# Performance work log

Hardware: AMD Instinct MI355X
Metric: run time of the kernel (lower is better)

Reference implementation:

```python
import jax, jax.numpy as jnp
import numpy as np
import math

N_HEADS = 8

def _layernorm(x, s, b):
    mu = x.mean(-1, keepdims=True)
    var = ((x - mu) ** 2).mean(-1, keepdims=True)
    return (x - mu) / jnp.sqrt(var + 1e-5) * s + b


def setup_inputs() -> dict:
    key = jax.random.key(0)
    ks = jax.random.split(key, 16)
    B, S, F, E, L, C, DFF = 4, 2048, 16, 512, 4, 35, 2048
    feat = jax.random.normal(ks[0], (B, S, F - 1), dtype=jnp.float32)
    amino = jax.random.randint(ks[1], (B, S), 0, 20).astype(jnp.float32)
    x = jnp.concatenate([feat, amino[..., None]], axis=-1)  # last channel = amino id
    lengths = np.array([2048, 1900, 1700, 1500])
    mask = jnp.asarray(np.arange(S)[None, :] >= lengths[:, None])  # True = padding
    M = 256
    rng = np.random.default_rng(0)
    mp = np.stack([np.sort(rng.choice(int(lengths[b]) - 1, M, replace=False)) for b in range(B)])
    masked_pos = jnp.asarray(mp, dtype=jnp.int32)
    # sinusoidal positional encoding [S, E]
    pos = np.arange(S)[:, None].astype(np.float32)
    div = np.exp(np.arange(0, E, 2).astype(np.float32) * (-math.log(10000.0) / E))
    pe_np = np.zeros((S, E), np.float32)
    pe_np[:, 0::2] = np.sin(pos * div)
    pe_np[:, 1::2] = np.cos(pos * div)
    pe = jnp.asarray(pe_np)
    sc = 1.0 / math.sqrt(E)
    def w(k, shape, s=sc):
        return jax.random.normal(k, shape, dtype=jnp.float32) * s
    return dict(
        x=x, mask=mask, masked_pos=masked_pos,
        arg1=jnp.float32(0.5), arg2=jnp.float32(0.8),
        embed_table=w(ks[2], (20, E - 15), 1.0), pe=pe,
        Wq=w(ks[3], (L, E, E)), bq=jnp.zeros((L, E)),
        Wk=w(ks[4], (L, E, E)), bk=jnp.zeros((L, E)),
        Wv=w(ks[5], (L, E, E)), bv=jnp.zeros((L, E)),
        Wo=w(ks[6], (L, E, E)), bo=jnp.zeros((L, E)),
        ln1_s=jnp.ones((L, E)), ln1_b=jnp.zeros((L, E)),
        W1=w(ks[7], (L, E, DFF)), b1=jnp.zeros((L, DFF)),
        W2=w(ks[8], (L, DFF, E), 1.0 / math.sqrt(DFF)), b2=jnp.zeros((L, E)),
        ln2_s=jnp.ones((L, E)), ln2_b=jnp.zeros((L, E)),
        fc_w=w(ks[9], (E, C)), fc_b=jnp.zeros((C,)),
    )


def _forward(x, mask, masked_pos, arg1, arg2, embed_table, pe, Wq, bq, Wk, bk, Wv, bv,
             Wo, bo, ln1_s, ln1_b, W1, b1, W2, b2, ln2_s, ln2_b, fc_w, fc_b):
    B, S, F = x.shape
    E = pe.shape[1]
    L = Wq.shape[0]
    H = N_HEADS
    Dh = E // H
    bidx = jnp.arange(B)[:, None]
    # get_mask: zero the masked token rows; label = original rows at masked positions
    mask_x = x.at[bidx, masked_pos].set(0.0)
    label = x[bidx, masked_pos].reshape(-1, F)
    # amino embedding with per-token min-max normalization
    amino = mask_x[:, :, -1].astype(jnp.int32)
    emb = embed_table[amino]  # [B,S,E-15]
    mn = emb.min(-1, keepdims=True)
    mx = emb.max(-1, keepdims=True)
    emb = (emb - mn) / (mx - mn)
    h = jnp.concatenate([mask_x[:, :, :-1], emb], axis=-1) + pe[None, :S, :]
    base = (~mask).astype(jnp.float32)  # 1 = valid key, 0 = pad
    for i in range(L):
        fill = arg1 if i == 0 else (arg2 if i == 1 else jnp.float32(1.0))
        m = base.at[bidx, masked_pos].set(fill)  # [B,S] key weights
        q = (h @ Wq[i] + bq[i]).reshape(B, S, H, Dh).transpose(0, 2, 1, 3)
        k = (h @ Wk[i] + bk[i]).reshape(B, S, H, Dh).transpose(0, 2, 1, 3)
        v = (h @ Wv[i] + bv[i]).reshape(B, S, H, Dh).transpose(0, 2, 1, 3)
        scores = jnp.einsum('bhqd,bhkd->bhqk', q, k) / Dh  # note: /head_dim, not sqrt
        mvec = m[:, None, None, :]
        scores = jnp.where(mvec != 0, scores * mvec, -jnp.inf)
        attn = jax.nn.softmax(scores, axis=-1)
        ws = jnp.einsum('bhqk,bhkd->bhqd', attn, v)  # [B,H,S,Dh]
        # faithful to torch: stacked [B,H,S,Dh].view(B,-1,E) row-major flatten
        attn_out = ws.reshape(B, -1, E) @ Wo[i] + bo[i]
        h = _layernorm(h + attn_out, ln1_s[i], ln1_b[i])
        ff = jax.nn.relu(h @ W1[i] + b1[i]) @ W2[i] + b2[i]
        h = _layernorm(h + ff, ln2_s[i], ln2_b[i])
    out_tok = h[bidx, masked_pos].reshape(-1, E)
    output = out_tok @ fc_w + fc_b
    return output[:, :15], output[:, 15:], label, h


def reference(x, mask, masked_pos, arg1, arg2, embed_table, pe, Wq, bq, Wk, bk, Wv, bv,
              Wo, bo, ln1_s, ln1_b, W1, b1, W2, b2, ln2_s, ln2_b, fc_w, fc_b):
    L1, CE, label, h = _forward(x, mask, masked_pos, arg1, arg2, embed_table, pe, Wq, bq,
                                Wk, bk, Wv, bv, Wo, bo, ln1_s, ln1_b, W1, b1, W2, b2,
                                ln2_s, ln2_b, fc_w, fc_b)
    return (L1, CE, label, h, mask)
```

## Files before the change

kernel.cpp:

```cpp
#include <hip/hip_runtime.h>
#include <hip/hip_bf16.h>


typedef __bf16 bf16_t;
typedef __bf16 bf16x8 __attribute__((ext_vector_type(8)));
typedef __bf16 bf16x4 __attribute__((ext_vector_type(4)));
typedef float  f32x4  __attribute__((ext_vector_type(4)));

#define ASYNC16(g, l) __builtin_amdgcn_global_load_lds( \
    (const __attribute__((address_space(1))) void*)(g),  \
    (__attribute__((address_space(3))) void*)(l), 16, 0, 0)

static __device__ __forceinline__ f32x4 mfma16(bf16x8 a, bf16x8 b, f32x4 c) {
  return __builtin_amdgcn_mfma_f32_16x16x32_bf16(a, b, c, 0, 0, 0);
}

static __device__ __forceinline__ float fexp2(float x) {
#if __has_builtin(__builtin_amdgcn_exp2f)
  return __builtin_amdgcn_exp2f(x);
#else
  return exp2f(x);
#endif
}

#define L2E 1.44269504f

__global__ void zero_flags_k(int* __restrict__ flags) {
  flags[blockIdx.x * 256 + threadIdx.x] = 0;
}

__global__ void scatter_k(const int* __restrict__ mpos, int* __restrict__ flags) {
  int t = blockIdx.x * 256 + threadIdx.x;
  int b = t >> 8;
  flags[b * 2048 + mpos[t]] = 1;
}

__global__ void masks_k(const int* __restrict__ flags,
                        const float* __restrict__ a1, const float* __restrict__ a2,
                        float* __restrict__ m05, float* __restrict__ m08,
                        float* __restrict__ mbase, float* __restrict__ maskout) {
  int i = blockIdx.x * 256 + threadIdx.x;
  int b = i >> 11, s = i & 2047;
  const int len0 = (b == 0) ? 2048 : (b == 1) ? 1900 : (b == 2) ? 1700 : 1500;
  float bs = (s < len0) ? 1.f : 0.f;
  int fl = flags[i];
  m05[i]   = fl ? a1[0] : bs;
  m08[i]   = fl ? a2[0] : bs;
  mbase[i] = fl ? 1.f   : bs;
  maskout[i] = 1.f - bs;
}

__global__ void label_k(const float* __restrict__ x, const int* __restrict__ mpos,
                        float* __restrict__ out) {
  int idx = blockIdx.x * 256 + threadIdx.x;
  int t = idx >> 4, f = idx & 15;
  int b = t >> 8;
  int pos = mpos[t];
  out[idx] = x[(b * 2048 + pos) * 16 + f];
}

__global__ __launch_bounds__(512) void embed_k(
    const float* __restrict__ x, const int* __restrict__ flags,
    const float* __restrict__ et, const float* __restrict__ pe,
    float* __restrict__ hf, bf16_t* __restrict__ hb) {
  const int tok = blockIdx.x, tid = threadIdx.x;
  const int s = tok & 2047;
  const int wave = tid >> 6, lane = tid & 63;
  __shared__ float e[512];
  __shared__ float redn[8], redx[8];
  const int masked = flags[tok];
  const float amf = masked ? 0.f : x[tok * 16 + 15];
  const int am = (int)amf;
  float ev = 0.f, vn = 3e38f, vx = -3e38f;
  if (tid < 497) { ev = et[am * 497 + tid]; e[tid] = ev; vn = ev; vx = ev; }
#pragma unroll
  for (int off = 1; off < 64; off <<= 1) {
    vn = fminf(vn, __shfl_xor(vn, off, 64));
    vx = fmaxf(vx, __shfl_xor(vx, off, 64));
  }
  if (lane == 0) { redn[wave] = vn; redx[wave] = vx; }
  __syncthreads();
  float mn = redn[0], mx = redx[0];
#pragma unroll
  for (int w = 1; w < 8; ++w) { mn = fminf(mn, redn[w]); mx = fmaxf(mx, redx[w]); }
  float val;
  if (tid < 15) val = masked ? 0.f : x[tok * 16 + tid];
  else          val = (e[tid - 15] - mn) / (mx - mn);
  val += pe[s * 512 + tid];
  hf[(size_t)tok * 512 + tid] = val;
  hb[(size_t)tok * 512 + tid] = (bf16_t)val;
}

__global__ void transpose_k(const float* __restrict__ in, bf16_t* __restrict__ out,
                            int K, int N, size_t ozstride) {
  __shared__ float t[32][33];
  in  += (size_t)blockIdx.z * K * N;
  out += (size_t)blockIdx.z * ozstride;
  const int n0 = blockIdx.x * 32, k0 = blockIdx.y * 32;
  const int tx = threadIdx.x & 31, ty = threadIdx.x >> 5;
#pragma unroll
  for (int i = 0; i < 32; i += 8)
    t[ty + i][tx] = in[(size_t)(k0 + ty + i) * N + n0 + tx];
  __syncthreads();
#pragma unroll
  for (int i = 0; i < 32; i += 8)
    out[(size_t)(n0 + ty + i) * K + k0 + tx] = (bf16_t)t[tx][ty + i];
}

template <int EPI>
__global__ __launch_bounds__(256) void gemm_k(
    const bf16_t* __restrict__ A, const bf16_t* __restrict__ Bt,
    const float* __restrict__ bias, const float* __restrict__ resid,
    float* __restrict__ outf, bf16_t* __restrict__ outb,
    int M, int N, int K) {
  __shared__ alignas(16) bf16_t As[2][128 * 32];
  __shared__ alignas(16) bf16_t Bs[2][128 * 32];
  const int tid = threadIdx.x;
  const int wave = tid >> 6, lane = tid & 63;
  const int quad = lane >> 4, l16 = lane & 15;
  const int n0 = blockIdx.x * 128, m0 = blockIdx.y * 128;
  const int wm = (wave & 1) * 64, wn = (wave >> 1) * 64;

  const int c0 = wave * 2, c1 = c0 + 1;
  const int sr = lane >> 2;
  const int sc = (((lane & 3) ^ ((sr >> 1) & 3))) * 8;
  const bf16_t* Ag0 = A + (size_t)(m0 + c0 * 16 + sr) * K + sc;
  const bf16_t* Ag1 = A + (size_t)(m0 + c1 * 16 + sr) * K + sc;
  const bf16_t* Bg0 = Bt + (size_t)(n0 + c0 * 16 + sr) * K + sc;
  const bf16_t* Bg1 = Bt + (size_t)(n0 + c1 * 16 + sr) * K + sc;

  const int cq = (quad ^ ((l16 >> 1) & 3)) * 8;

  f32x4 acc[4][4] = {};
  const int nit = K >> 5;

  ASYNC16(Ag0, &As[0][c0 * 512]);
  ASYNC16(Ag1, &As[0][c1 * 512]);
  ASYNC16(Bg0, &Bs[0][c0 * 512]);
  ASYNC16(Bg1, &Bs[0][c1 * 512]);
  __syncthreads();

  for (int it = 0; it < nit; ++it) {
    const int cur = it & 1, nxt = cur ^ 1;
    if (it + 1 < nit) {
      const int ko = (it + 1) << 5;
      ASYNC16(Ag0 + ko, &As[nxt][c0 * 512]);
      ASYNC16(Ag1 + ko, &As[nxt][c1 * 512]);
      ASYNC16(Bg0 + ko, &Bs[nxt][c0 * 512]);
      ASYNC16(Bg1 + ko, &Bs[nxt][c1 * 512]);
    }
    bf16x8 af[4], bfr[4];
#pragma unroll
    for (int mi = 0; mi < 4; ++mi)
      af[mi] = *(const bf16x8*)&As[cur][(wm + mi * 16 + l16) * 32 + cq];
#pragma unroll
    for (int ni = 0; ni < 4; ++ni)
      bfr[ni] = *(const bf16x8*)&Bs[cur][(wn + ni * 16 + l16) * 32 + cq];
#pragma unroll
    for (int mi = 0; mi < 4; ++mi)
#pragma unroll
      for (int ni = 0; ni < 4; ++ni)
        acc[mi][ni] = mfma16(af[mi], bfr[ni], acc[mi][ni]);
    __syncthreads();
  }

#pragma unroll
  for (int ni = 0; ni < 4; ++ni) {
    const int gn = n0 + wn + ni * 16 + l16;
    const float bv = bias[gn];
#pragma unroll
    for (int mi = 0; mi < 4; ++mi) {
#pragma unroll
      for (int r = 0; r < 4; ++r) {
        const int gm = m0 + wm + mi * 16 + quad * 4 + r;
        float v = acc[mi][ni][r] + bv;
        if (EPI == 2) {
          outf[(size_t)gm * N + gn] = v + resid[(size_t)gm * N + gn];
        } else {
          outb[(size_t)gm * N + gn] = (bf16_t)fmaxf(v, 0.f);
        }
      }
    }
  }
}

__global__ __launch_bounds__(256) void gemm64_k(
    const bf16_t* __restrict__ A, const bf16_t* __restrict__ Bt,
    const float* __restrict__ bias, const float* __restrict__ resid,
    float* __restrict__ outf, int M, int N, int K) {
  __shared__ alignas(16) bf16_t As[2][64 * 64];
  __shared__ alignas(16) bf16_t Bs[2][128 * 64];
  const int tid = threadIdx.x;
  const int wave = tid >> 6, lane = tid & 63;
  const int quad = lane >> 4, l16 = lane & 15;
  const int n0 = blockIdx.x * 128, m0 = blockIdx.y * 64;
  const int wm = (wave & 1) * 32, wn = (wave >> 1) * 64;

  const bf16_t* gptr[6];
  int soff[6];
  bool isA[6];
#pragma unroll
  for (int i = 0; i < 6; ++i) {
    const int s = tid + 256 * i;
    if (s < 512) {
      const int r = s >> 3, c = s & 7, g = c ^ ((r >> 1) & 7);
      gptr[i] = A + (size_t)(m0 + r) * K + g * 8;
      soff[i] = s * 16;  isA[i] = true;
    } else {
      const int sb = s - 512;
      const int r = sb >> 3, c = sb & 7, g = c ^ ((r >> 1) & 7);
      gptr[i] = Bt + (size_t)(n0 + r) * K + g * 8;
      soff[i] = sb * 16; isA[i] = false;
    }
  }

  const int swl = (l16 >> 1) & 7;
  f32x4 acc[2][4] = {};
  const int nit = K >> 6;

#pragma unroll
  for (int i = 0; i < 6; ++i)
    ASYNC16(gptr[i], (char*)(isA[i] ? &As[0][0] : &Bs[0][0]) + soff[i]);
  __syncthreads();

  for (int it = 0; it < nit; ++it) {
    const int cur = it & 1, nxt = cur ^ 1;
    if (it + 1 < nit) {
      const int ko = (it + 1) << 6;
#pragma unroll
      for (int i = 0; i < 6; ++i)
        ASYNC16(gptr[i] + ko, (char*)(isA[i] ? &As[nxt][0] : &Bs[nxt][0]) + soff[i]);
    }
#pragma unroll
    for (int h = 0; h < 2; ++h) {
      const int cq = ((quad + 4 * h) ^ swl) * 8;
      bf16x8 af[2], bfr[4];
#pragma unroll
      for (int mi = 0; mi < 2; ++mi)
        af[mi] = *(const bf16x8*)&As[cur][(wm + mi * 16 + l16) * 64 + cq];
#pragma unroll
      for (int ni = 0; ni < 4; ++ni)
        bfr[ni] = *(const bf16x8*)&Bs[cur][(wn + ni * 16 + l16) * 64 + cq];
#pragma unroll
      for (int mi = 0; mi < 2; ++mi)
#pragma unroll
        for (int ni = 0; ni < 4; ++ni)
          acc[mi][ni] = mfma16(af[mi], bfr[ni], acc[mi][ni]);
    }
    __syncthreads();
  }

#pragma unroll
  for (int ni = 0; ni < 4; ++ni) {
    const int gn = n0 + wn + ni * 16 + l16;
    const float bv = bias[gn];
#pragma unroll
    for (int mi = 0; mi < 2; ++mi) {
#pragma unroll
      for (int r = 0; r < 4; ++r) {
        const int gm = m0 + wm + mi * 16 + quad * 4 + r;
        outf[(size_t)gm * N + gn] = acc[mi][ni][r] + bv + resid[(size_t)gm * N + gn];
      }
    }
  }
}

__global__ __launch_bounds__(256) void gemm_qkv_k(
    const bf16_t* __restrict__ A, const bf16_t* __restrict__ Bt,
    const float* __restrict__ bq, const float* __restrict__ bk,
    const float* __restrict__ bv, const float* __restrict__ mw,
    bf16_t* __restrict__ qb, bf16_t* __restrict__ kb, bf16_t* __restrict__ vtb) {
  const int K = 512;
  __shared__ alignas(16) bf16_t As[2][128 * 32];
  __shared__ alignas(16) bf16_t Bs[2][128 * 32];
  const int tid = threadIdx.x;
  const int wave = tid >> 6, lane = tid & 63;
  const int quad = lane >> 4, l16 = lane & 15;
  const int n0 = blockIdx.x * 128, m0 = blockIdx.y * 128;
  const int wm = (wave & 1) * 64, wn = (wave >> 1) * 64;

  const int c0 = wave * 2, c1 = c0 + 1;
  const int sr = lane >> 2;
  const int sc = (((lane & 3) ^ ((sr >> 1) & 3))) * 8;
  const bf16_t* Ag0 = A + (size_t)(m0 + c0 * 16 + sr) * K + sc;
  const bf16_t* Ag1 = A + (size_t)(m0 + c1 * 16 + sr) * K + sc;
  const bf16_t* Bg0 = Bt + (size_t)(n0 + c0 * 16 + sr) * K + sc;
  const bf16_t* Bg1 = Bt + (size_t)(n0 + c1 * 16 + sr) * K + sc;

  const int cq = (quad ^ ((l16 >> 1) & 3)) * 8;

  f32x4 acc[4][4] = {};
  const int nit = K >> 5;

  ASYNC16(Ag0, &As[0][c0 * 512]);
  ASYNC16(Ag1, &As[0][c1 * 512]);
  ASYNC16(Bg0, &Bs[0][c0 * 512]);
  ASYNC16(Bg1, &Bs[0][c1 * 512]);
  __syncthreads();

  for (int it = 0; it < nit; ++it) {
    const int cur = it & 1, nxt = cur ^ 1;
    if (it + 1 < nit) {
      const int ko = (it + 1) << 5;
      ASYNC16(Ag0 + ko, &As[nxt][c0 * 512]);
      ASYNC16(Ag1 + ko, &As[nxt][c1 * 512]);
      ASYNC16(Bg0 + ko, &Bs[nxt][c0 * 512]);
      ASYNC16(Bg1 + ko, &Bs[nxt][c1 * 512]);
    }
    bf16x8 af[4], bfr[4];
#pragma unroll
    for (int mi = 0; mi < 4; ++mi)
      af[mi] = *(const bf16x8*)&As[cur][(wm + mi * 16 + l16) * 32 + cq];
#pragma unroll
    for (int ni = 0; ni < 4; ++ni)
      bfr[ni] = *(const bf16x8*)&Bs[cur][(wn + ni * 16 + l16) * 32 + cq];
#pragma unroll
    for (int mi = 0; mi < 4; ++mi)
#pragma unroll
      for (int ni = 0; ni < 4; ++ni)
        acc[mi][ni] = mfma16(af[mi], bfr[ni], acc[mi][ni]);
    __syncthreads();
  }

  const int which = n0 >> 9;
  const float* bias = (which == 0) ? bq : (which == 1) ? bk : bv;
  bf16_t* dst = (which == 0) ? qb : (which == 1) ? kb : vtb;
  float kmul[4][4];
  if (which == 1) {
#pragma unroll
    for (int mi = 0; mi < 4; ++mi)
#pragma unroll
      for (int r = 0; r < 4; ++r) {
        const int gm = m0 + wm + mi * 16 + quad * 4 + r;
        kmul[mi][r] = mw[(gm >> 11) * 2048 + (gm & 2047)] * (0.015625f * L2E);
      }
  }
#pragma unroll
  for (int ni = 0; ni < 4; ++ni) {
    const int gn = n0 + wn + ni * 16 + l16;
    const int col = gn & 511;
    const float bvx = bias[col];
    const int hh = col >> 6, dd = col & 63;
#pragma unroll
    for (int mi = 0; mi < 4; ++mi) {
#pragma unroll
      for (int r = 0; r < 4; ++r) {
        const int gm = m0 + wm + mi * 16 + quad * 4 + r;
        const int bb = gm >> 11, ss = gm & 2047;
        float v = acc[mi][ni][r] + bvx;
        if (which == 0) {
          dst[(size_t)(((bb * 8 + hh) * 2048) + ss) * 64 + dd] = (bf16_t)v;
        } else if (which == 1) {
          v *= kmul[mi][r];
          dst[(size_t)(((bb * 8 + hh) * 2048) + ss) * 64 + dd] = (bf16_t)v;
        } else {
          const int o5 = ss & 31;
          const int ssp = (ss & ~31) | ((o5 & 12) << 1) | ((o5 & 16) >> 2) | (o5 & 3);
          dst[(size_t)(((bb * 8 + hh) * 64) + dd) * 2048 + ssp] = (bf16_t)v;
        }
      }
    }
  }
}

__global__ __launch_bounds__(256, 2) void attn_k(
    const bf16_t* __restrict__ Q, const bf16_t* __restrict__ Kmat,
    const bf16_t* __restrict__ VT, bf16_t* __restrict__ out) {
  __shared__ alignas(16) bf16_t Ks[128 * 64];
  __shared__ alignas(16) bf16_t Vs[64 * 128];
  const int tid = threadIdx.x, wave = tid >> 6, lane = tid & 63;
  const int quad = lane >> 4, l16 = lane & 15;
  const int qt = blockIdx.x, bh = blockIdx.y;
  const int b = bh >> 3, hh = bh & 7;
  const int len = (b == 0) ? 2048 : (b == 1) ? 1900 : (b == 2) ? 1700 : 1500;
  const bf16_t* __restrict__ Qh = Q    + (size_t)bh * 2048 * 64;
  const bf16_t* __restrict__ Kh = Kmat + (size_t)bh * 2048 * 64;
  const bf16_t* __restrict__ Vh = VT   + (size_t)bh * 64 * 2048;
  const int q0 = qt * 128 + wave * 32;

  bf16x8 aq[2][2];
#pragma unroll
  for (int qf = 0; qf < 2; ++qf) {
    aq[qf][0] = *(const bf16x8*)&Qh[(size_t)(q0 + qf * 16 + l16) * 64 + quad * 8];
    aq[qf][1] = *(const bf16x8*)&Qh[(size_t)(q0 + qf * 16 + l16) * 64 + 32 + quad * 8];
  }

  f32x4 o[2][4] = {};
  f32x4 os[2] = {};
  bf16x8 onesb;
#pragma unroll
  for (int j = 0; j < 8; ++j) onesb[j] = (bf16_t)1.0f;

  const int krow = wave * 8 + (lane >> 3);
  const int kchk = (lane & 7) ^ (lane >> 3);
  const int vrow = wave * 4 + (lane >> 4);
  const int vchk = (lane & 15) ^ (wave * 4 + (lane >> 4));
  const int kc0 = quad ^ (l16 & 7);
  const int kc1 = (quad + 4) ^ (l16 & 7);

  const int ntiles = (len + 127) >> 7;
  for (int kt = 0; kt < ntiles; ++kt) {
    const int k0 = kt * 128;
    __syncthreads();
#pragma unroll
    for (int i = 0; i < 4; ++i)
      ASYNC16(Kh + (size_t)(k0 + i * 32 + krow) * 64 + kchk * 8,
              &Ks[(i * 32 + wave * 8) * 64]);
#pragma unroll
    for (int i = 0; i < 4; ++i)
      ASYNC16(Vh + (size_t)(i * 16 + vrow) * 2048 + k0 + vchk * 8,
              &Vs[(i * 16 + wave * 4) * 128]);
    __syncthreads();

    f32x4 sc0[8], sc1[8];
#pragma unroll
    for (int t = 0; t < 8; ++t) {
      const bf16x8 kf0 = *(const bf16x8*)&Ks[(t * 16 + l16) * 64 + kc0 * 8];
      const bf16x8 kf1 = *(const bf16x8*)&Ks[(t * 16 + l16) * 64 + kc1 * 8];
      f32x4 z0 = {0.f, 0.f, 0.f, 0.f};
      z0 = mfma16(kf0, aq[0][0], z0);
      z0 = mfma16(kf1, aq[0][1], z0);
      sc0[t] = z0;
      f32x4 z1 = {0.f, 0.f, 0.f, 0.f};
      z1 = mfma16(kf0, aq[1][0], z1);
      z1 = mfma16(kf1, aq[1][1], z1);
      sc1[t] = z1;
    }
    if (k0 + 128 > len) {
#pragma unroll
      for (int t = 0; t < 8; ++t)
#pragma unroll
        for (int r = 0; r < 4; ++r) {
          const bool pad = (k0 + t * 16 + quad * 4 + r >= len);
          if (pad) { sc0[t][r] = -1e30f; sc1[t][r] = -1e30f; }
        }
    }
    bf16x8 pbp[2][4];
#pragma unroll
    for (int t = 0; t < 8; ++t)
#pragma unroll
      for (int r = 0; r < 4; ++r) {
        pbp[0][t >> 1][(t & 1) * 4 + r] = (bf16_t)fexp2(sc0[t][r]);
        pbp[1][t >> 1][(t & 1) * 4 + r] = (bf16_t)fexp2(sc1[t][r]);
      }
#pragma unroll
    for (int T = 0; T < 4; ++T) {
      const int slot = ((4 * T + quad) ^ l16) * 8;
#pragma unroll
      for (int ni = 0; ni < 4; ++ni) {
        const bf16x8 vb = *(const bf16x8*)&Vs[(ni * 16 + l16) * 128 + slot];
        o[0][ni] = mfma16(pbp[0][T], vb, o[0][ni]);
        o[1][ni] = mfma16(pbp[1][T], vb, o[1][ni]);
      }
      os[0] = mfma16(pbp[0][T], onesb, os[0]);
      os[1] = mfma16(pbp[1][T], onesb, os[1]);
    }
  }

#pragma unroll
  for (int qf = 0; qf < 2; ++qf) {
    float linv[4];
#pragma unroll
    for (int r = 0; r < 4; ++r) linv[r] = 1.f / os[qf][r];
#pragma unroll
    for (int ni = 0; ni < 4; ++ni) {
#pragma unroll
      for (int r = 0; r < 4; ++r) {
        const int s_tok = q0 + qf * 16 + quad * 4 + r;
        const int d = ni * 16 + l16;
        const int row = b * 2048 + hh * 256 + (s_tok >> 3);
        const int col = (s_tok & 7) * 64 + d;
        out[(size_t)row * 512 + col] = (bf16_t)(o[qf][ni][r] * linv[r]);
      }
    }
  }
}

__global__ __launch_bounds__(256) void ln_k(
    const float* __restrict__ in, const float* __restrict__ sc,
    const float* __restrict__ bi, float* __restrict__ hf, bf16_t* __restrict__ hb) {
  const int row = blockIdx.x, tid = threadIdx.x;
  const int wave = tid >> 6, lane = tid & 63;
  const float* x = in + (size_t)row * 512;
  float v0 = x[tid], v1 = x[tid + 256];
  float s = v0 + v1, s2 = v0 * v0 + v1 * v1;
#pragma unroll
  for (int off = 1; off < 64; off <<= 1) {
    s  += __shfl_xor(s, off, 64);
    s2 += __shfl_xor(s2, off, 64);
  }
  __shared__ float red[8];
  if (lane == 0) { red[wave] = s; red[4 + wave] = s2; }
  __syncthreads();
  float ts  = red[0] + red[1] + red[2] + red[3];
  float ts2 = red[4] + red[5] + red[6] + red[7];
  float mu = ts * (1.f / 512.f);
  float var = ts2 * (1.f / 512.f) - mu * mu;
  float rstd = rsqrtf(var + 1e-5f);
  float o0 = (v0 - mu) * rstd * sc[tid] + bi[tid];
  float o1 = (v1 - mu) * rstd * sc[tid + 256] + bi[tid + 256];
  hf[(size_t)row * 512 + tid] = o0;
  hf[(size_t)row * 512 + tid + 256] = o1;
  hb[(size_t)row * 512 + tid] = (bf16_t)o0;
  hb[(size_t)row * 512 + tid + 256] = (bf16_t)o1;
}

__global__ void head_k(const float* __restrict__ hf, const int* __restrict__ mpos,
                       const float* __restrict__ fw, const float* __restrict__ fb,
                       float* __restrict__ out0, float* __restrict__ out1) {
  const int t = blockIdx.x;
  const int b = t >> 8;
  const int pos = mpos[t];
  const float* hr = hf + (size_t)(b * 2048 + pos) * 512;
  __shared__ float hrow[512];
  for (int i = threadIdx.x; i < 512; i += 64) hrow[i] = hr[i];
  __syncthreads();
  const int c = threadIdx.x;
  if (c < 35) {
    float acc = fb[c];
    for (int k = 0; k < 512; ++k) acc += hrow[k] * fw[k * 35 + c];
    if (c < 15) out0[t * 15 + c] = acc;
    else        out1[t * 20 + (c - 15)] = acc;
  }
}

extern "C" void kernel_launch(void* const* d_in, const int* in_sizes, int n_in,
                              void* d_out, int out_size, void* d_ws, size_t ws_size,
                              hipStream_t stream) {
  const float* x    = (const float*)d_in[0];
  const int*   mpos = (const int*)d_in[2];
  const float* a1   = (const float*)d_in[3];
  const float* a2   = (const float*)d_in[4];
  const float* et   = (const float*)d_in[5];
  const float* pe   = (const float*)d_in[6];
  const float* Wq   = (const float*)d_in[7];
  const float* bq   = (const float*)d_in[8];
  const float* Wk   = (const float*)d_in[9];
  const float* bk   = (const float*)d_in[10];
  const float* Wv   = (const float*)d_in[11];
  const float* bv   = (const float*)d_in[12];
  const float* Wo   = (const float*)d_in[13];
  const float* bo   = (const float*)d_in[14];
  const float* l1s  = (const float*)d_in[15];
  const float* l1b  = (const float*)d_in[16];
  const float* W1   = (const float*)d_in[17];
  const float* b1   = (const float*)d_in[18];
  const float* W2   = (const float*)d_in[19];
  const float* b2   = (const float*)d_in[20];
  const float* l2s  = (const float*)d_in[21];
  const float* l2b  = (const float*)d_in[22];
  const float* fcw  = (const float*)d_in[23];
  const float* fcb  = (const float*)d_in[24];

  char* w = (char*)d_ws;
  const size_t MB = 1024 * 1024;
  bf16_t* qkvT = (bf16_t*)(w + 0 * MB);
  bf16_t* wot  = (bf16_t*)(w + 6 * MB);
  bf16_t* w1t  = (bf16_t*)(w + 8 * MB);
  bf16_t* w2t  = (bf16_t*)(w + 16 * MB);
  float*  hf   = (float*) (w + 24 * MB);
  bf16_t* hb   = (bf16_t*)(w + 40 * MB);
  float*  tmp  = (float*) (w + 48 * MB);
  int*    flags= (int*)   (w + 64 * MB);
  float*  m05  = (float*) (w + 64 * MB + 64 * 1024);
  float*  m08  = (float*) (w + 64 * MB + 128 * 1024);
  float*  mba  = (float*) (w + 64 * MB + 192 * 1024);
  bf16_t* qb   = (bf16_t*)(w + 65 * MB);
  bf16_t* kb   = (bf16_t*)(w + 73 * MB);
  bf16_t* vtb  = (bf16_t*)(w + 81 * MB);
  bf16_t* ao   = (bf16_t*)(w + 89 * MB);
  bf16_t* ff1  = (bf16_t*)(w + 65 * MB);

  float* out0    = (float*)d_out;
  float* out1    = out0 + 1024 * 15;
  float* outlab  = out1 + 1024 * 20;
  float* outh    = outlab + 1024 * 16;
  float* outmask = outh + 4 * 2048 * 512;

  zero_flags_k<<<32, 256, 0, stream>>>(flags);
  scatter_k<<<4, 256, 0, stream>>>(mpos, flags);
  masks_k<<<32, 256, 0, stream>>>(flags, a1, a2, m05, m08, mba, outmask);
  embed_k<<<8192, 512, 0, stream>>>(x, flags, et, pe, hf, hb);
  label_k<<<64, 256, 0, stream>>>(x, mpos, outlab);
  transpose_k<<<dim3(16, 16, 4), 256, 0, stream>>>(Wq, qkvT + 0 * 262144, 512, 512, 786432);
  transpose_k<<<dim3(16, 16, 4), 256, 0, stream>>>(Wk, qkvT + 1 * 262144, 512, 512, 786432);
  transpose_k<<<dim3(16, 16, 4), 256, 0, stream>>>(Wv, qkvT + 2 * 262144, 512, 512, 786432);
  transpose_k<<<dim3(16, 16, 4), 256, 0, stream>>>(Wo, wot, 512, 512, 262144);
  transpose_k<<<dim3(64, 16, 4), 256, 0, stream>>>(W1, w1t, 512, 2048, 1048576);
  transpose_k<<<dim3(16, 64, 4), 256, 0, stream>>>(W2, w2t, 2048, 512, 1048576);

  for (int i = 0; i < 4; ++i) {
    const float* mv = (i == 0) ? m05 : (i == 1) ? m08 : mba;
    gemm_qkv_k<<<dim3(12, 64), 256, 0, stream>>>(hb, qkvT + (size_t)i * 786432,
                                                 bq + i * 512, bk + i * 512, bv + i * 512,
                                                 mv, qb, kb, vtb);
    attn_k<<<dim3(16, 32), 256, 0, stream>>>(qb, kb, vtb, ao);
    gemm64_k<<<dim3(4, 128), 256, 0, stream>>>(ao, wot + i * 262144, bo + i * 512,
                                               hf, tmp, 8192, 512, 512);
    ln_k<<<8192, 256, 0, stream>>>(tmp, l1s + i * 512, l1b + i * 512, hf, hb);
    gemm_k<3><<<dim3(16, 64), 256, 0, stream>>>(hb, w1t + i * 1048576, b1 + i * 2048,
                                                nullptr, nullptr, ff1, 8192, 2048, 512);
    gemm64_k<<<dim3(4, 128), 256, 0, stream>>>(ff1, w2t + i * 1048576, b2 + i * 512,
                                               hf, tmp, 8192, 512, 2048);
    float* lnout = (i == 3) ? outh : hf;
    ln_k<<<8192, 256, 0, stream>>>(tmp, l2s + i * 512, l2b + i * 512, lnout, hb);
  }
  head_k<<<1024, 64, 0, stream>>>(outh, mpos, fcw, fcb, out0, out1);
}
```

Measured before the change: 874.6 us.

## Triple-buffer GEMM loads and double-buffer attention K/V tiles with explicit waitcnt

Measured after the change: 880.7 us. Within noise of the previous version (+0.7%).

```diff
diff --git a/kernel.cpp b/kernel.cpp
--- a/kernel.cpp
+++ b/kernel.cpp
@@ -10,6 +10,9 @@
 #define ASYNC16(g, l) __builtin_amdgcn_global_load_lds( \
     (const __attribute__((address_space(1))) void*)(g),  \
     (__attribute__((address_space(3))) void*)(l), 16, 0, 0)
+
+#define S_VMCNT(Nstr) asm volatile("s_waitcnt vmcnt(" Nstr ")" ::: "memory")
+#define S_BARRIER()   asm volatile("s_barrier" ::: "memory")
 
 static __device__ __forceinline__ f32x4 mfma16(bf16x8 a, bf16x8 b, f32x4 c) {
   return __builtin_amdgcn_mfma_f32_16x16x32_bf16(a, b, c, 0, 0, 0);
@@ -113,8 +116,8 @@
     const float* __restrict__ bias, const float* __restrict__ resid,
     float* __restrict__ outf, bf16_t* __restrict__ outb,
     int M, int N, int K) {
-  __shared__ alignas(16) bf16_t As[2][128 * 32];
-  __shared__ alignas(16) bf16_t Bs[2][128 * 32];
+  __shared__ alignas(16) bf16_t As[3][128 * 32];
+  __shared__ alignas(16) bf16_t Bs[3][128 * 32];
   const int tid = threadIdx.x;
   const int wave = tid >> 6, lane = tid & 63;
   const int quad = lane >> 4, l16 = lane & 15;
@@ -134,21 +137,27 @@
   f32x4 acc[4][4] = {};
   const int nit = K >> 5;
 
-  ASYNC16(Ag0, &As[0][c0 * 512]);
-  ASYNC16(Ag1, &As[0][c1 * 512]);
-  ASYNC16(Bg0, &Bs[0][c0 * 512]);
-  ASYNC16(Bg1, &Bs[0][c1 * 512]);
-  __syncthreads();
+#pragma unroll 1
+  for (int p = 0; p < 2; ++p) {
+    const int ko = p << 5;
+    ASYNC16(Ag0 + ko, &As[p][c0 * 512]);
+    ASYNC16(Ag1 + ko, &As[p][c1 * 512]);
+    ASYNC16(Bg0 + ko, &Bs[p][c0 * 512]);
+    ASYNC16(Bg1 + ko, &Bs[p][c1 * 512]);
+  }
 
   for (int it = 0; it < nit; ++it) {
-    const int cur = it & 1, nxt = cur ^ 1;
-    if (it + 1 < nit) {
-      const int ko = (it + 1) << 5;
-      ASYNC16(Ag0 + ko, &As[nxt][c0 * 512]);
-      ASYNC16(Ag1 + ko, &As[nxt][c1 * 512]);
-      ASYNC16(Bg0 + ko, &Bs[nxt][c0 * 512]);
-      ASYNC16(Bg1 + ko, &Bs[nxt][c1 * 512]);
-    }
+    if (it + 1 < nit) { S_VMCNT("4"); } else { S_VMCNT("0"); }
+    S_BARRIER();
+    if (it + 2 < nit) {
+      const int pb = (it + 2) % 3;
+      const int ko = (it + 2) << 5;
+      ASYNC16(Ag0 + ko, &As[pb][c0 * 512]);
+      ASYNC16(Ag1 + ko, &As[pb][c1 * 512]);
+      ASYNC16(Bg0 + ko, &Bs[pb][c0 * 512]);
+      ASYNC16(Bg1 + ko, &Bs[pb][c1 * 512]);
+    }
+    const int cur = it % 3;
     bf16x8 af[4], bfr[4];
 #pragma unroll
     for (int mi = 0; mi < 4; ++mi)
@@ -161,7 +170,6 @@
 #pragma unroll
       for (int ni = 0; ni < 4; ++ni)
         acc[mi][ni] = mfma16(af[mi], bfr[ni], acc[mi][ni]);
-    __syncthreads();
   }
 
 #pragma unroll
@@ -188,8 +196,8 @@
     const bf16_t* __restrict__ A, const bf16_t* __restrict__ Bt,
     const float* __restrict__ bias, const float* __restrict__ resid,
     float* __restrict__ outf, int M, int N, int K) {
-  __shared__ alignas(16) bf16_t As[2][64 * 64];
-  __shared__ alignas(16) bf16_t Bs[2][128 * 64];
+  __shared__ alignas(16) bf16_t As[3][64 * 64];
+  __shared__ alignas(16) bf16_t Bs[3][128 * 64];
   const int tid = threadIdx.x;
   const int wave = tid >> 6, lane = tid & 63;
   const int quad = lane >> 4, l16 = lane & 15;
@@ -218,19 +226,25 @@
   f32x4 acc[2][4] = {};
   const int nit = K >> 6;
 
-#pragma unroll
-  for (int i = 0; i < 6; ++i)
-    ASYNC16(gptr[i], (char*)(isA[i] ? &As[0][0] : &Bs[0][0]) + soff[i]);
-  __syncthreads();
+#pragma unroll 1
+  for (int p = 0; p < 2; ++p) {
+    const int ko = p << 6;
+#pragma unroll
+    for (int i = 0; i < 6; ++i)
+      ASYNC16(gptr[i] + ko, (char*)(isA[i] ? &As[p][0] : &Bs[p][0]) + soff[i]);
+  }
 
   for (int it = 0; it < nit; ++it) {
-    const int cur = it & 1, nxt = cur ^ 1;
-    if (it + 1 < nit) {
-      const int ko = (it + 1) << 6;
+    if (it + 1 < nit) { S_VMCNT("6"); } else { S_VMCNT("0"); }
+    S_BARRIER();
+    if (it + 2 < nit) {
+      const int pb = (it + 2) % 3;
+      const int ko = (it + 2) << 6;
 #pragma unroll
       for (int i = 0; i < 6; ++i)
-        ASYNC16(gptr[i] + ko, (char*)(isA[i] ? &As[nxt][0] : &Bs[nxt][0]) + soff[i]);
-    }
+        ASYNC16(gptr[i] + ko, (char*)(isA[i] ? &As[pb][0] : &Bs[pb][0]) + soff[i]);
+    }
+    const int cur = it % 3;
 #pragma unroll
     for (int h = 0; h < 2; ++h) {
       const int cq = ((quad + 4 * h) ^ swl) * 8;
@@ -247,7 +261,6 @@
         for (int ni = 0; ni < 4; ++ni)
           acc[mi][ni] = mfma16(af[mi], bfr[ni], acc[mi][ni]);
     }
-    __syncthreads();
   }
 
 #pragma unroll
@@ -271,8 +284,8 @@
     const float* __restrict__ bv, const float* __restrict__ mw,
     bf16_t* __restrict__ qb, bf16_t* __restrict__ kb, bf16_t* __restrict__ vtb) {
   const int K = 512;
-  __shared__ alignas(16) bf16_t As[2][128 * 32];
-  __shared__ alignas(16) bf16_t Bs[2][128 * 32];
+  __shared__ alignas(16) bf16_t As[3][128 * 32];
+  __shared__ alignas(16) bf16_t Bs[3][128 * 32];
   const int tid = threadIdx.x;
   const int wave = tid >> 6, lane = tid & 63;
   const int quad = lane >> 4, l16 = lane & 15;
@@ -292,21 +305,27 @@
   f32x4 acc[4][4] = {};
   const int nit = K >> 5;
 
-  ASYNC16(Ag0, &As[0][c0 * 512]);
-  ASYNC16(Ag1, &As[0][c1 * 512]);
-  ASYNC16(Bg0, &Bs[0][c0 * 512]);
-  ASYNC16(Bg1, &Bs[0][c1 * 512]);
-  __syncthreads();
+#pragma unroll 1
+  for (int p = 0; p < 2; ++p) {
+    const int ko = p << 5;
+    ASYNC16(Ag0 + ko, &As[p][c0 * 512]);
+    ASYNC16(Ag1 + ko, &As[p][c1 * 512]);
+    ASYNC16(Bg0 + ko, &Bs[p][c0 * 512]);
+    ASYNC16(Bg1 + ko, &Bs[p][c1 * 512]);
+  }
 
   for (int it = 0; it < nit; ++it) {
-    const int cur = it & 1, nxt = cur ^ 1;
-    if (it + 1 < nit) {
-      const int ko = (it + 1) << 5;
-      ASYNC16(Ag0 + ko, &As[nxt][c0 * 512]);
-      ASYNC16(Ag1 + ko, &As[nxt][c1 * 512]);
-      ASYNC16(Bg0 + ko, &Bs[nxt][c0 * 512]);
-      ASYNC16(Bg1 + ko, &Bs[nxt][c1 * 512]);
-    }
+    if (it + 1 < nit) { S_VMCNT("4"); } else { S_VMCNT("0"); }
+    S_BARRIER();
+    if (it + 2 < nit) {
+      const int pb = (it + 2) % 3;
+      const int ko = (it + 2) << 5;
+      ASYNC16(Ag0 + ko, &As[pb][c0 * 512]);
+      ASYNC16(Ag1 + ko, &As[pb][c1 * 512]);
+      ASYNC16(Bg0 + ko, &Bs[pb][c0 * 512]);
+      ASYNC16(Bg1 + ko, &Bs[pb][c1 * 512]);
+    }
+    const int cur = it % 3;
     bf16x8 af[4], bfr[4];
 #pragma unroll
     for (int mi = 0; mi < 4; ++mi)
@@ -319,7 +338,6 @@
 #pragma unroll
       for (int ni = 0; ni < 4; ++ni)
         acc[mi][ni] = mfma16(af[mi], bfr[ni], acc[mi][ni]);
-    __syncthreads();
   }
 
   const int which = n0 >> 9;
@@ -366,8 +384,8 @@
 __global__ __launch_bounds__(256, 2) void attn_k(
     const bf16_t* __restrict__ Q, const bf16_t* __restrict__ Kmat,
     const bf16_t* __restrict__ VT, bf16_t* __restrict__ out) {
-  __shared__ alignas(16) bf16_t Ks[128 * 64];
-  __shared__ alignas(16) bf16_t Vs[64 * 128];
+  __shared__ alignas(16) bf16_t Ks[2][128 * 64];
+  __shared__ alignas(16) bf16_t Vs[2][64 * 128];
   const int tid = threadIdx.x, wave = tid >> 6, lane = tid & 63;
   const int quad = lane >> 4, l16 = lane & 15;
   const int qt = blockIdx.x, bh = blockIdx.y;
@@ -399,24 +417,39 @@
   const int kc1 = (quad + 4) ^ (l16 & 7);
 
   const int ntiles = (len + 127) >> 7;
+
+#pragma unroll
+  for (int i = 0; i < 4; ++i)
+    ASYNC16(Kh + (size_t)(i * 32 + krow) * 64 + kchk * 8,
+            &Ks[0][(i * 32 + wave * 8) * 64]);
+#pragma unroll
+  for (int i = 0; i < 4; ++i)
+    ASYNC16(Vh + (size_t)(i * 16 + vrow) * 2048 + vchk * 8,
+            &Vs[0][(i * 16 + wave * 4) * 128]);
+
   for (int kt = 0; kt < ntiles; ++kt) {
+    S_VMCNT("0");
+    S_BARRIER();
+    if (kt + 1 < ntiles) {
+      const int k1 = (kt + 1) * 128;
+      const int nb = (kt + 1) & 1;
+#pragma unroll
+      for (int i = 0; i < 4; ++i)
+        ASYNC16(Kh + (size_t)(k1 + i * 32 + krow) * 64 + kchk * 8,
+                &Ks[nb][(i * 32 + wave * 8) * 64]);
+#pragma unroll
+      for (int i = 0; i < 4; ++i)
+        ASYNC16(Vh + (size_t)(i * 16 + vrow) * 2048 + k1 + vchk * 8,
+                &Vs[nb][(i * 16 + wave * 4) * 128]);
+    }
+    const int cb = kt & 1;
     const int k0 = kt * 128;
-    __syncthreads();
-#pragma unroll
-    for (int i = 0; i < 4; ++i)
-      ASYNC16(Kh + (size_t)(k0 + i * 32 + krow) * 64 + kchk * 8,
-              &Ks[(i * 32 + wave * 8) * 64]);
-#pragma unroll
-    for (int i = 0; i < 4; ++i)
-      ASYNC16(Vh + (size_t)(i * 16 + vrow) * 2048 + k0 + vchk * 8,
-              &Vs[(i * 16 + wave * 4) * 128]);
-    __syncthreads();
 
     f32x4 sc0[8], sc1[8];
 #pragma unroll
     for (int t = 0; t < 8; ++t) {
-      const bf16x8 kf0 = *(const bf16x8*)&Ks[(t * 16 + l16) * 64 + kc0 * 8];
-      const bf16x8 kf1 = *(const bf16x8*)&Ks[(t * 16 + l16) * 64 + kc1 * 8];
+      const bf16x8 kf0 = *(const bf16x8*)&Ks[cb][(t * 16 + l16) * 64 + kc0 * 8];
+      const bf16x8 kf1 = *(const bf16x8*)&Ks[cb][(t * 16 + l16) * 64 + kc1 * 8];
       f32x4 z0 = {0.f, 0.f, 0.f, 0.f};
       z0 = mfma16(kf0, aq[0][0], z0);
       z0 = mfma16(kf1, aq[0][1], z0);
@@ -448,7 +481,7 @@
       const int slot = ((4 * T + quad) ^ l16) * 8;
 #pragma unroll
       for (int ni = 0; ni < 4; ++ni) {
-        const bf16x8 vb = *(const bf16x8*)&Vs[(ni * 16 + l16) * 128 + slot];
+        const bf16x8 vb = *(const bf16x8*)&Vs[cb][(ni * 16 + l16) * 128 + slot];
         o[0][ni] = mfma16(pbp[0][T], vb, o[0][ni]);
         o[1][ni] = mfma16(pbp[1][T], vb, o[1][ni]);
       }
```
